# Kernel optimization log

Hardware: AMD Instinct MI355X
Metric: run time of the kernel (lower is better)

The kernel has to match this reference:

```python
import jax, jax.numpy as jnp
import numpy as np

KP_EXTENT = 1.2  # influence radius of each kernel point (init arg KP_extent)
SHADOW_COORD = 1e6  # shadow point coordinate for padding (as in original KPConv)


def setup_inputs() -> dict:
    key = jax.random.key(0)
    k1, k2, k3, k4, k5, k6 = jax.random.split(key, 6)
    N, Ns, H, K, Cin, Cout = 20000, 20000, 40, 15, 128, 128
    q_pts = jax.random.uniform(k1, (N, 3), dtype=jnp.float32)
    s_pts = jax.random.uniform(k2, (Ns, 3), dtype=jnp.float32)
    neighb_inds = jax.random.randint(k3, (N, H), 0, Ns, dtype=jnp.int32)
    x = jax.random.normal(k4, (Ns, Cin), dtype=jnp.float32)
    # kernel point positions inside the sphere (stand-in for load_kernels output)
    kernel_points = jax.random.normal(k5, (K, 3), dtype=jnp.float32) * 0.5
    kernel_points = kernel_points.at[0].set(0.0)  # fixed='center'
    weights = jax.random.normal(k6, (K, Cin, Cout), dtype=jnp.float32) * (1.0 / np.sqrt(Cin))
    return {"q_pts": q_pts, "s_pts": s_pts, "neighb_inds": neighb_inds,
            "x": x, "kernel_points": kernel_points, "weights": weights}


def reference(q_pts, s_pts, neighb_inds, x, kernel_points, weights):
    # Pad support points with a far-away shadow point and features with a zero row,
    # so out-of-range neighbor index Ns contributes nothing (original KPConv trick).
    s_pad = jnp.concatenate([s_pts, jnp.full((1, s_pts.shape[1]), SHADOW_COORD, s_pts.dtype)], axis=0)
    x_pad = jnp.concatenate([x, jnp.zeros((1, x.shape[1]), x.dtype)], axis=0)

    # Gather neighbor coords, center on query points: [N, H, 3]
    neighbors = s_pad[neighb_inds] - q_pts[:, None, :]

    # Squared distance to every kernel point: [N, H, K]
    diff = neighbors[:, :, None, :] - kernel_points[None, None, :, :]
    sq_dist = jnp.sum(diff * diff, axis=-1)

    # Linear influence weights, aggregation_mode='sum': [N, K, H]
    all_weights = jnp.clip(1.0 - jnp.sqrt(sq_dist) / KP_EXTENT, 0.0, None)
    all_weights = jnp.swapaxes(all_weights, 1, 2)

    # Gather neighbor features: [N, H, Cin]
    neighb_x = x_pad[neighb_inds]

    # Influence-weighted aggregation over neighbors: [N, K, Cin]
    weighted = jnp.einsum('nkh,nhc->nkc', all_weights, neighb_x)

    # Per-kernel-point linear maps, summed over kernel points: [N, Cout]
    out = jnp.einsum('nkc,kcd->nd', weighted, weights)
    return out
```

## Files before the change

kernel.cpp:

```cpp
#include <hip/hip_runtime.h>

#define KP   15
#define HN   40
#define CIN  128
#define COUT 128
#define KDIM (KP*CIN)
#define KP_EXT_INV (1.0f/1.2f)

typedef __bf16 bf16x8 __attribute__((ext_vector_type(8)));
typedef __bf16 bf16x4 __attribute__((ext_vector_type(4)));
typedef float  f32x4  __attribute__((ext_vector_type(4)));

__device__ inline void async_copy16(const void* g, void* lds) {
    __builtin_amdgcn_global_load_lds(
        (const __attribute__((address_space(1))) unsigned int*)g,
        (__attribute__((address_space(3))) unsigned int*)lds, 16, 0, 0);
}

__global__ __launch_bounds__(256)
void kpconv_prep(const float* __restrict__ x, const float* __restrict__ W,
                 __bf16* __restrict__ xb, __bf16* __restrict__ Wt,
                 int nx_elems, int nxB)
{
    __shared__ float sW[32][133];
    const int b = blockIdx.x;
    const int t = threadIdx.x;

    if (b < nxB) {
        const int e0 = (b*256 + t) * 8;
        if (e0 + 8 <= nx_elems) {
            const float4 f0 = *(const float4*)(x + e0);
            const float4 f1 = *(const float4*)(x + e0 + 4);
            bf16x8 v;
            v[0]=(__bf16)f0.x; v[1]=(__bf16)f0.y; v[2]=(__bf16)f0.z; v[3]=(__bf16)f0.w;
            v[4]=(__bf16)f1.x; v[5]=(__bf16)f1.y; v[6]=(__bf16)f1.z; v[7]=(__bf16)f1.w;
            *(bf16x8*)(xb + e0) = v;
        } else {
            for (int e = e0; e < nx_elems; ++e) xb[e] = (__bf16)x[e];
        }
    } else {
        const int kc0 = (b - nxB) * 32;
        #pragma unroll
        for (int i = 0; i < 4; ++i) {
            const int off = t*4 + i*1024;
            const int r = off >> 7, c = off & 127;
            const float4 f = *(const float4*)(W + (size_t)(kc0 + r)*COUT + c);
            sW[r][c+0]=f.x; sW[r][c+1]=f.y; sW[r][c+2]=f.z; sW[r][c+3]=f.w;
        }
        __syncthreads();
        #pragma unroll
        for (int i = 0; i < 2; ++i) {
            const int id = t + i*256;
            const int d  = id >> 2, ch = id & 3;
            bf16x8 v;
            #pragma unroll
            for (int j = 0; j < 8; ++j) v[j] = (__bf16)sW[ch*8 + j][d];
            *(bf16x8*)(Wt + (size_t)d*KDIM + kc0 + ch*8) = v;
        }
    }
}

__global__ __launch_bounds__(256, 4)
void kpconv_aggregate(const float* __restrict__ q_pts,
                      const float* __restrict__ s_pts,
                      const int*   __restrict__ nb,
                      const __bf16* __restrict__ xb,
                      const float* __restrict__ kpts,
                      __bf16* __restrict__ wsA,
                      int N, int Ns)
{
    __shared__ __align__(16) __bf16 sXt[4][4][128][8];
    __shared__ __align__(16) float4 s_nd[4][HN];
    __shared__ int                  s_idx[4][HN];

    const int t  = threadIdx.x;
    const int wv = t >> 6;
    const int l  = t & 63;
    const int m  = l & 15;
    const int q  = l >> 4;
    const int n  = blockIdx.x * 4 + wv;

    if (l < HN) {
        int idx = nb[n*HN + l];
        float dx, dy, dz;
        if (idx >= 0 && idx < Ns) {
            dx = s_pts[idx*3+0] - q_pts[n*3+0];
            dy = s_pts[idx*3+1] - q_pts[n*3+1];
            dz = s_pts[idx*3+2] - q_pts[n*3+2];
        } else { idx = 0; dx = dy = dz = 2.0e6f; }
        s_idx[wv][l] = idx;
        s_nd[wv][l]  = make_float4(dx, dy, dz, 0.f);
    }
    __asm__ __volatile__("s_waitcnt lgkmcnt(0)" ::: "memory");

    float kx = 0.f, ky = 0.f, kz = 0.f;
    if (m < KP) { kx = kpts[m*3+0]; ky = kpts[m*3+1]; kz = kpts[m*3+2]; }

    bf16x8 wfrag[2];
    #pragma unroll
    for (int ks = 0; ks < 2; ++ks) {
        #pragma unroll
        for (int j = 0; j < 8; ++j) {
            const int h = ks*32 + q*8 + j;
            float w = 0.f;
            if (m < KP && h < HN) {
                float4 nd = s_nd[wv][h];
                float dx = nd.x - kx, dy = nd.y - ky, dz = nd.z - kz;
                w = fmaxf(1.0f - sqrtf(dx*dx + dy*dy + dz*dz)*KP_EXT_INV, 0.f);
            }
            wfrag[ks][j] = (__bf16)w;
        }
    }

    f32x4 acc[8];
    #pragma unroll
    for (int nt = 0; nt < 8; ++nt) acc[nt] = (f32x4){0.f,0.f,0.f,0.f};

    #pragma unroll
    for (int ks = 0; ks < 2; ++ks) {
        const int iters = ks ? 1 : 4;
        #pragma unroll
        for (int it = 0; it < iters; ++it) {
            const int hp = ks*16 + it*4 + q;
            const int h0 = 2*hp;
            const uint4 a  = *(const uint4*)(xb + (size_t)s_idx[wv][h0  ]*CIN + m*8);
            const uint4 bb = *(const uint4*)(xb + (size_t)s_idx[wv][h0+1]*CIN + m*8);
            const unsigned av[4] = {a.x, a.y, a.z, a.w};
            const unsigned bv[4] = {bb.x, bb.y, bb.z, bb.w};
            const int hl = h0 - ks*32;
            const int hc = hl >> 3;
            const int dw = hp & 3;
            unsigned* plane = (unsigned*)&sXt[wv][hc][0][0];
            #pragma unroll
            for (int j = 0; j < 8; ++j) {
                const unsigned v = __builtin_amdgcn_perm(
                    bv[j>>1], av[j>>1], (j&1) ? 0x07060302u : 0x05040100u);
                const int p = m*8 + (j ^ (m & 7));
                plane[p*4 + dw] = v;
            }
        }
        __asm__ __volatile__("s_waitcnt lgkmcnt(0)" ::: "memory");

        #pragma unroll
        for (int nt = 0; nt < 8; ++nt) {
            const int cc = nt*16 + m;
            const int p  = (cc & ~7) | ((cc & 7) ^ ((cc >> 3) & 7));
            bf16x8 xf = *(const bf16x8*)&sXt[wv][q][p][0];
            acc[nt] = __builtin_amdgcn_mfma_f32_16x16x32_bf16(
                          xf, wfrag[ks], acc[nt], 0, 0, 0);
        }
    }

    if (m < KP) {
        #pragma unroll
        for (int nt = 0; nt < 8; ++nt) {
            bf16x4 v;
            #pragma unroll
            for (int r = 0; r < 4; ++r) v[r] = (__bf16)acc[nt][r];
            *(bf16x4*)(wsA + (size_t)n*KDIM + m*CIN + nt*16 + q*4) = v;
        }
    }
}

#define BM 64
#define BK 128

__global__ __launch_bounds__(256, 3)
void kpconv_gemm(const __bf16* __restrict__ A,
                 const __bf16* __restrict__ Bt,
                 float* __restrict__ out, int M)
{
    __shared__ __align__(16) __bf16 sA[BM*BK];
    __shared__ __align__(16) __bf16 sB[COUT*BK];

    const int t     = threadIdx.x;
    const int wv    = t >> 6;
    const int l     = t & 63;
    const int mlane = l & 15;
    const int q     = l >> 4;
    const int m0    = blockIdx.x * BM;

    const int rA = t >> 4;
    const int pA = t & 15;

    f32x4 acc[4][2];
    #pragma unroll
    for (int i = 0; i < 4; ++i)
        #pragma unroll
        for (int j = 0; j < 2; ++j) acc[i][j] = (f32x4){0.f,0.f,0.f,0.f};

    for (int k0 = 0; k0 < KDIM; k0 += BK) {
        #pragma unroll
        for (int pass = 0; pass < 4; ++pass) {
            const int r  = rA + pass*16;
            int rg = m0 + r; if (rg >= M) rg = M - 1;
            const int ch = pA ^ (r & 15);
            async_copy16(A + (size_t)rg*KDIM + k0 + ch*8,
                         (char*)sA + pass*4096 + wv*1024 + l*16);
        }
        #pragma unroll
        for (int pass = 0; pass < 8; ++pass) {
            const int r  = rA + pass*16;
            const int ch = pA ^ (r & 15);
            async_copy16(Bt + (size_t)r*KDIM + k0 + ch*8,
                         (char*)sB + pass*4096 + wv*1024 + l*16);
        }
        __syncthreads();

        #pragma unroll
        for (int ksi = 0; ksi < 4; ++ksi) {
            bf16x8 af[4], bfr[2];
            #pragma unroll
            for (int mt = 0; mt < 4; ++mt) {
                const int row = mt*16 + mlane;
                const int p   = (ksi*4 + q) ^ (row & 15);
                af[mt] = *(const bf16x8*)&sA[row*BK + p*8];
            }
            #pragma unroll
            for (int j = 0; j < 2; ++j) {
                const int row = (wv*2 + j)*16 + mlane;
                const int p   = (ksi*4 + q) ^ (row & 15);
                bfr[j] = *(const bf16x8*)&sB[row*BK + p*8];
            }
            #pragma unroll
            for (int mt = 0; mt < 4; ++mt)
                #pragma unroll
                for (int j = 0; j < 2; ++j)
                    acc[mt][j] = __builtin_amdgcn_mfma_f32_16x16x32_bf16(
                                     af[mt], bfr[j], acc[mt][j], 0, 0, 0);
        }
        __syncthreads();
    }

    #pragma unroll
    for (int mt = 0; mt < 4; ++mt)
        #pragma unroll
        for (int j = 0; j < 2; ++j)
            #pragma unroll
            for (int r = 0; r < 4; ++r) {
                const int row = m0 + mt*16 + q*4 + r;
                if (row < M)
                    out[(size_t)row*COUT + (wv*2+j)*16 + mlane] = acc[mt][j][r];
            }
}

#define TM 8
#define WSTR (KP*CIN + 4)

__global__ __launch_bounds__(256, 2)
void kpconv_fused(const float* __restrict__ q_pts,
                  const float* __restrict__ s_pts,
                  const int*   __restrict__ nb,
                  const float* __restrict__ x,
                  const float* __restrict__ kpts,
                  const float* __restrict__ W,
                  float* __restrict__ out,
                  int N, int Ns)
{
    __shared__ float s_kp[KP*3];
    __shared__ float s_nd2[HN*3];
    __shared__ int   s_idx2[HN];
    __shared__ float s_w[KP][HN];
    __shared__ float s_wt[TM*WSTR];

    const int t  = threadIdx.x;
    const int n0 = (int)blockIdx.x * TM;
    if (t < KP*3) s_kp[t] = kpts[t];
    const int c = t & (CIN-1);
    const int g = t >> 7;

    for (int mm = 0; mm < TM; ++mm) {
        const int n = n0 + mm;
        if (t < HN) {
            float dx = 1e6f, dy = 1e6f, dz = 1e6f;
            int idx = 0;
            if (n < N) {
                idx = nb[n*HN + t];
                if (idx >= 0 && idx < Ns) {
                    dx = s_pts[idx*3+0] - q_pts[n*3+0];
                    dy = s_pts[idx*3+1] - q_pts[n*3+1];
                    dz = s_pts[idx*3+2] - q_pts[n*3+2];
                } else idx = 0;
            }
            s_idx2[t] = idx;
            s_nd2[t*3+0] = dx; s_nd2[t*3+1] = dy; s_nd2[t*3+2] = dz;
        }
        __syncthreads();
        for (int task = t; task < KP*HN; task += 256) {
            const int k = task / HN;
            const int h = task - k*HN;
            const float dx = s_nd2[h*3+0] - s_kp[k*3+0];
            const float dy = s_nd2[h*3+1] - s_kp[k*3+1];
            const float dz = s_nd2[h*3+2] - s_kp[k*3+2];
            s_w[k][h] = fmaxf(1.0f - sqrtf(dx*dx+dy*dy+dz*dz)*KP_EXT_INV, 0.0f);
        }
        __syncthreads();
        float facc[8];
        #pragma unroll
        for (int j = 0; j < 8; ++j) facc[j] = 0.0f;
        #pragma unroll 8
        for (int h = 0; h < HN; ++h) {
            const float xv = x[s_idx2[h]*CIN + c];
            #pragma unroll
            for (int j = 0; j < 8; ++j) {
                const int k = g + 2*j;
                if (k < KP) facc[j] += s_w[k][h] * xv;
            }
        }
        #pragma unroll
        for (int j = 0; j < 8; ++j) {
            const int k = g + 2*j;
            if (k < KP) s_wt[mm*WSTR + k*CIN + c] = facc[j];
        }
        __syncthreads();
    }

    const int m3 = t >> 5;
    const int d0 = (t & 31) * 4;
    const float* wm = &s_wt[m3*WSTR];
    float ax = 0.f, ay = 0.f, az = 0.f, aw = 0.f;
    #pragma unroll 4
    for (int kc = 0; kc < KP*CIN; ++kc) {
        const float  wvv = wm[kc];
        const float4 wr = *(const float4*)&W[kc*COUT + d0];
        ax += wvv * wr.x; ay += wvv * wr.y; az += wvv * wr.z; aw += wvv * wr.w;
    }
    const int n = n0 + m3;
    if (n < N) {
        float4 o; o.x = ax; o.y = ay; o.z = az; o.w = aw;
        *(float4*)&out[n*COUT + d0] = o;
    }
}

extern "C" void kernel_launch(void* const* d_in, const int* in_sizes, int n_in,
                              void* d_out, int out_size, void* d_ws, size_t ws_size,
                              hipStream_t stream) {
    const float* q_pts = (const float*)d_in[0];
    const float* s_pts = (const float*)d_in[1];
    const int*   nb    = (const int*)  d_in[2];
    const float* x     = (const float*)d_in[3];
    const float* kpts  = (const float*)d_in[4];
    const float* W     = (const float*)d_in[5];
    float* out = (float*)d_out;

    const int N  = in_sizes[0] / 3;
    const int Ns = in_sizes[1] / 3;
    const int nx = in_sizes[3];

    const size_t needA = (size_t)N * KDIM * sizeof(__bf16);
    const size_t needB = (size_t)COUT * KDIM * sizeof(__bf16);
    const size_t needX = (size_t)nx * sizeof(__bf16);

    if (ws_size >= needA + needB + needX && (N % 4) == 0 && (KDIM % 128) == 0) {
        __bf16* wsA = (__bf16*)d_ws;
        __bf16* wsB = (__bf16*)((char*)d_ws + needA);
        __bf16* wsX = (__bf16*)((char*)d_ws + needA + needB);

        const int nxB = (nx/8 + 255) / 256;
        const int nwB = KDIM / 32;
        hipLaunchKernelGGL(kpconv_prep, dim3(nxB + nwB), dim3(256), 0, stream,
                           x, W, wsX, wsB, nx, nxB);
        hipLaunchKernelGGL(kpconv_aggregate, dim3(N/4), dim3(256), 0, stream,
                           q_pts, s_pts, nb, wsX, kpts, wsA, N, Ns);
        hipLaunchKernelGGL(kpconv_gemm, dim3((N + BM - 1)/BM), dim3(256), 0, stream,
                           wsA, wsB, out, N);
    } else {
        const int grid = (N + TM - 1) / TM;
        hipLaunchKernelGGL(kpconv_fused, dim3(grid), dim3(256), 0, stream,
                           q_pts, s_pts, nb, x, kpts, W, out, N, Ns);
    }
}
```

Measured before the change: 148.2 us.

## Process two points per wave with prefetched gathers; shrink GEMM tile, read B from registers

The aggregate kernel now handles two query points per wave. It issues all neighbor feature gathers for both points up front into registers, so their latency overlaps the influence-weight computation, and it rewrites the squared distance as a precomputed-norm fma form using a fast sqrt. The GEMM drops its LDS staging of the weight matrix, loading B fragments straight from global memory (expected to hit L2), and halves the M tile to 32 rows so more blocks run. The costs are higher register pressure in the aggregate kernel (launch bounds lowered to 3), repeated global reads of B per block, and a new requirement that N be divisible by 32.

```diff
diff --git a/kernel.cpp b/kernel.cpp
--- a/kernel.cpp
+++ b/kernel.cpp
@@ -16,6 +16,7 @@
         (const __attribute__((address_space(1))) unsigned int*)g,
         (__attribute__((address_space(3))) unsigned int*)lds, 16, 0, 0);
 }
+#define LGKM0() __asm__ __volatile__("s_waitcnt lgkmcnt(0)" ::: "memory")
 
 __global__ __launch_bounds__(256)
 void kpconv_prep(const float* __restrict__ x, const float* __restrict__ W,
@@ -60,7 +61,7 @@
     }
 }
 
-__global__ __launch_bounds__(256, 4)
+__global__ __launch_bounds__(256, 3)
 void kpconv_aggregate(const float* __restrict__ q_pts,
                       const float* __restrict__ s_pts,
                       const int*   __restrict__ nb,
@@ -70,178 +71,195 @@
                       int N, int Ns)
 {
     __shared__ __align__(16) __bf16 sXt[4][4][128][8];
-    __shared__ __align__(16) float4 s_nd[4][HN];
-    __shared__ int                  s_idx[4][HN];
+    __shared__ __align__(16) float4 s_nd[4][2][HN];
+    __shared__ int                  s_idx[4][2][HN];
 
     const int t  = threadIdx.x;
     const int wv = t >> 6;
     const int l  = t & 63;
     const int m  = l & 15;
     const int q  = l >> 4;
-    const int n  = blockIdx.x * 4 + wv;
-
-    if (l < HN) {
-        int idx = nb[n*HN + l];
-        float dx, dy, dz;
-        if (idx >= 0 && idx < Ns) {
-            dx = s_pts[idx*3+0] - q_pts[n*3+0];
-            dy = s_pts[idx*3+1] - q_pts[n*3+1];
-            dz = s_pts[idx*3+2] - q_pts[n*3+2];
-        } else { idx = 0; dx = dy = dz = 2.0e6f; }
-        s_idx[wv][l] = idx;
-        s_nd[wv][l]  = make_float4(dx, dy, dz, 0.f);
-    }
-    __asm__ __volatile__("s_waitcnt lgkmcnt(0)" ::: "memory");
-
-    float kx = 0.f, ky = 0.f, kz = 0.f;
+    const int nbase = (blockIdx.x*4 + wv)*2;
+
+    #pragma unroll
+    for (int pp = 0; pp < 2; ++pp) {
+        if (l < HN) {
+            const int n = nbase + pp;
+            int idx = nb[n*HN + l];
+            float dx, dy, dz;
+            if (idx >= 0 && idx < Ns) {
+                dx = s_pts[idx*3+0] - q_pts[n*3+0];
+                dy = s_pts[idx*3+1] - q_pts[n*3+1];
+                dz = s_pts[idx*3+2] - q_pts[n*3+2];
+            } else { idx = 0; dx = dy = dz = 2.0e6f; }
+            s_idx[wv][pp][l] = idx;
+            s_nd[wv][pp][l]  = make_float4(dx, dy, dz, dx*dx + dy*dy + dz*dz);
+        }
+    }
+    LGKM0();
+
+    uint4 g[2][5][2];
+    #pragma unroll
+    for (int pp = 0; pp < 2; ++pp) {
+        #pragma unroll
+        for (int it = 0; it < 5; ++it) {
+            const int h0 = (it < 4) ? (it*8 + 2*q) : (32 + 2*q);
+            g[pp][it][0] = *(const uint4*)(xb + (size_t)s_idx[wv][pp][h0  ]*CIN + m*8);
+            g[pp][it][1] = *(const uint4*)(xb + (size_t)s_idx[wv][pp][h0+1]*CIN + m*8);
+        }
+    }
+
+    float kx=0.f, ky=0.f, kz=0.f;
     if (m < KP) { kx = kpts[m*3+0]; ky = kpts[m*3+1]; kz = kpts[m*3+2]; }
-
-    bf16x8 wfrag[2];
-    #pragma unroll
-    for (int ks = 0; ks < 2; ++ks) {
-        #pragma unroll
-        for (int j = 0; j < 8; ++j) {
-            const int h = ks*32 + q*8 + j;
-            float w = 0.f;
-            if (m < KP && h < HN) {
-                float4 nd = s_nd[wv][h];
-                float dx = nd.x - kx, dy = nd.y - ky, dz = nd.z - kz;
-                w = fmaxf(1.0f - sqrtf(dx*dx + dy*dy + dz*dz)*KP_EXT_INV, 0.f);
-            }
-            wfrag[ks][j] = (__bf16)w;
-        }
-    }
-
-    f32x4 acc[8];
-    #pragma unroll
-    for (int nt = 0; nt < 8; ++nt) acc[nt] = (f32x4){0.f,0.f,0.f,0.f};
-
-    #pragma unroll
-    for (int ks = 0; ks < 2; ++ks) {
-        const int iters = ks ? 1 : 4;
-        #pragma unroll
-        for (int it = 0; it < iters; ++it) {
-            const int hp = ks*16 + it*4 + q;
-            const int h0 = 2*hp;
-            const uint4 a  = *(const uint4*)(xb + (size_t)s_idx[wv][h0  ]*CIN + m*8);
-            const uint4 bb = *(const uint4*)(xb + (size_t)s_idx[wv][h0+1]*CIN + m*8);
-            const unsigned av[4] = {a.x, a.y, a.z, a.w};
-            const unsigned bv[4] = {bb.x, bb.y, bb.z, bb.w};
-            const int hl = h0 - ks*32;
-            const int hc = hl >> 3;
-            const int dw = hp & 3;
-            unsigned* plane = (unsigned*)&sXt[wv][hc][0][0];
+    const float kk  = kx*kx + ky*ky + kz*kz;
+    const float kx2 = -2.f*kx, ky2 = -2.f*ky, kz2 = -2.f*kz;
+
+    bf16x8 wfrag[2][2];
+    #pragma unroll
+    for (int pp = 0; pp < 2; ++pp) {
+        #pragma unroll
+        for (int ks = 0; ks < 2; ++ks) {
             #pragma unroll
             for (int j = 0; j < 8; ++j) {
-                const unsigned v = __builtin_amdgcn_perm(
-                    bv[j>>1], av[j>>1], (j&1) ? 0x07060302u : 0x05040100u);
-                const int p = m*8 + (j ^ (m & 7));
-                plane[p*4 + dw] = v;
-            }
-        }
-        __asm__ __volatile__("s_waitcnt lgkmcnt(0)" ::: "memory");
-
-        #pragma unroll
-        for (int nt = 0; nt < 8; ++nt) {
-            const int cc = nt*16 + m;
-            const int p  = (cc & ~7) | ((cc & 7) ^ ((cc >> 3) & 7));
-            bf16x8 xf = *(const bf16x8*)&sXt[wv][q][p][0];
-            acc[nt] = __builtin_amdgcn_mfma_f32_16x16x32_bf16(
-                          xf, wfrag[ks], acc[nt], 0, 0, 0);
-        }
-    }
-
-    if (m < KP) {
-        #pragma unroll
-        for (int nt = 0; nt < 8; ++nt) {
-            bf16x4 v;
-            #pragma unroll
-            for (int r = 0; r < 4; ++r) v[r] = (__bf16)acc[nt][r];
-            *(bf16x4*)(wsA + (size_t)n*KDIM + m*CIN + nt*16 + q*4) = v;
-        }
-    }
-}
-
-#define BM 64
-#define BK 128
-
-__global__ __launch_bounds__(256, 3)
+                const int h = ks*32 + q*8 + j;
+                float w = 0.f;
+                if (m < KP && h < HN) {
+                    const float4 nd = s_nd[wv][pp][h];
+                    const float d2 = fmaf(nd.x, kx2,
+                                     fmaf(nd.y, ky2,
+                                     fmaf(nd.z, kz2, nd.w + kk)));
+                    const float d = __builtin_amdgcn_sqrtf(d2);
+                    w = fmaxf(fmaf(d, -KP_EXT_INV, 1.0f), 0.f);
+                }
+                wfrag[pp][ks][j] = (__bf16)w;
+            }
+        }
+    }
+
+    #pragma unroll
+    for (int pp = 0; pp < 2; ++pp) {
+        const int n = nbase + pp;
+        f32x4 acc[8];
+        #pragma unroll
+        for (int nt = 0; nt < 8; ++nt) acc[nt] = (f32x4){0.f,0.f,0.f,0.f};
+
+        #pragma unroll
+        for (int ks = 0; ks < 2; ++ks) {
+            const int itBeg = ks ? 4 : 0;
+            const int itEnd = ks ? 5 : 4;
+            #pragma unroll
+            for (int it = itBeg; it < itEnd; ++it) {
+                const unsigned av[4] = {g[pp][it][0].x, g[pp][it][0].y,
+                                        g[pp][it][0].z, g[pp][it][0].w};
+                const unsigned bv[4] = {g[pp][it][1].x, g[pp][it][1].y,
+                                        g[pp][it][1].z, g[pp][it][1].w};
+                const int hc = ks ? 0 : it;
+                const int dw = q;
+                unsigned* plane = (unsigned*)&sXt[wv][hc][0][0];
+                #pragma unroll
+                for (int j = 0; j < 8; ++j) {
+                    const unsigned v = __builtin_amdgcn_perm(
+                        bv[j>>1], av[j>>1], (j&1) ? 0x07060302u : 0x05040100u);
+                    const int p = m*8 + (j ^ (m & 7));
+                    plane[p*4 + dw] = v;
+                }
+            }
+            LGKM0();
+
+            #pragma unroll
+            for (int nt = 0; nt < 8; ++nt) {
+                const int cc = nt*16 + m;
+                const int p  = (cc & ~7) | ((cc & 7) ^ ((cc >> 3) & 7));
+                bf16x8 xf = *(const bf16x8*)&sXt[wv][q][p][0];
+                acc[nt] = __builtin_amdgcn_mfma_f32_16x16x32_bf16(
+                              xf, wfrag[pp][ks], acc[nt], 0, 0, 0);
+            }
+        }
+
+        if (m < KP) {
+            #pragma unroll
+            for (int nt = 0; nt < 8; ++nt) {
+                bf16x4 v;
+                #pragma unroll
+                for (int r = 0; r < 4; ++r) v[r] = (__bf16)acc[nt][r];
+                *(bf16x4*)(wsA + (size_t)n*KDIM + m*CIN + nt*16 + q*4) = v;
+            }
+        }
+    }
+}
+
+#define GBM 32
+
+__global__ __launch_bounds__(256, 4)
 void kpconv_gemm(const __bf16* __restrict__ A,
                  const __bf16* __restrict__ Bt,
                  float* __restrict__ out, int M)
 {
-    __shared__ __align__(16) __bf16 sA[BM*BK];
-    __shared__ __align__(16) __bf16 sB[COUT*BK];
+    __shared__ __align__(16) __bf16 sA[GBM*128];
 
     const int t     = threadIdx.x;
     const int wv    = t >> 6;
     const int l     = t & 63;
     const int mlane = l & 15;
     const int q     = l >> 4;
-    const int m0    = blockIdx.x * BM;
-
-    const int rA = t >> 4;
-    const int pA = t & 15;
-
-    f32x4 acc[4][2];
-    #pragma unroll
-    for (int i = 0; i < 4; ++i)
+    const int m0    = blockIdx.x * GBM;
+
+    const int r0  = t >> 4;
+    const int pos = t & 15;
+
+    const __bf16* Brow0 = Bt + (size_t)(wv*32 + mlane) * KDIM;
+    const __bf16* Brow1 = Brow0 + (size_t)16 * KDIM;
+
+    f32x4 acc[2][2];
+    #pragma unroll
+    for (int i = 0; i < 2; ++i)
         #pragma unroll
         for (int j = 0; j < 2; ++j) acc[i][j] = (f32x4){0.f,0.f,0.f,0.f};
 
-    for (int k0 = 0; k0 < KDIM; k0 += BK) {
-        #pragma unroll
-        for (int pass = 0; pass < 4; ++pass) {
-            const int r  = rA + pass*16;
-            int rg = m0 + r; if (rg >= M) rg = M - 1;
-            const int ch = pA ^ (r & 15);
-            async_copy16(A + (size_t)rg*KDIM + k0 + ch*8,
-                         (char*)sA + pass*4096 + wv*1024 + l*16);
-        }
-        #pragma unroll
-        for (int pass = 0; pass < 8; ++pass) {
-            const int r  = rA + pass*16;
-            const int ch = pA ^ (r & 15);
-            async_copy16(Bt + (size_t)r*KDIM + k0 + ch*8,
-                         (char*)sB + pass*4096 + wv*1024 + l*16);
-        }
-        __syncthreads();
-
-        #pragma unroll
-        for (int ksi = 0; ksi < 4; ++ksi) {
-            bf16x8 af[4], bfr[2];
-            #pragma unroll
-            for (int mt = 0; mt < 4; ++mt) {
+    for (int k0 = 0; k0 < KDIM; k0 += 128) {
+        #pragma unroll
+        for (int p = 0; p < 2; ++p) {
+            const int row = r0 + p*16;
+            const int ch  = pos ^ (row & 15);
+            async_copy16(A + (size_t)(m0 + row)*KDIM + k0 + ch*8,
+                         (char*)sA + (p*256 + t)*16);
+        }
+        __syncthreads();
+
+        bf16x8 bfr[2][4];
+        #pragma unroll
+        for (int ks = 0; ks < 4; ++ks) {
+            bfr[0][ks] = *(const bf16x8*)(Brow0 + k0 + ks*32 + q*8);
+            bfr[1][ks] = *(const bf16x8*)(Brow1 + k0 + ks*32 + q*8);
+        }
+
+        #pragma unroll
+        for (int ks = 0; ks < 4; ++ks) {
+            bf16x8 af[2];
+            #pragma unroll
+            for (int mt = 0; mt < 2; ++mt) {
                 const int row = mt*16 + mlane;
-                const int p   = (ksi*4 + q) ^ (row & 15);
-                af[mt] = *(const bf16x8*)&sA[row*BK + p*8];
-            }
-            #pragma unroll
-            for (int j = 0; j < 2; ++j) {
-                const int row = (wv*2 + j)*16 + mlane;
-                const int p   = (ksi*4 + q) ^ (row & 15);
-                bfr[j] = *(const bf16x8*)&sB[row*BK + p*8];
-            }
-            #pragma unroll
-            for (int mt = 0; mt < 4; ++mt)
+                const int p   = (ks*4 + q) ^ (row & 15);
+                af[mt] = *(const bf16x8*)&sA[row*128 + p*8];
+            }
+            #pragma unroll
+            for (int mt = 0; mt < 2; ++mt)
                 #pragma unroll
                 for (int j = 0; j < 2; ++j)
                     acc[mt][j] = __builtin_amdgcn_mfma_f32_16x16x32_bf16(
-                                     af[mt], bfr[j], acc[mt][j], 0, 0, 0);
-        }
-        __syncthreads();
-    }
-
-    #pragma unroll
-    for (int mt = 0; mt < 4; ++mt)
+                                     af[mt], bfr[j][ks], acc[mt][j], 0, 0, 0);
+        }
+        __syncthreads();
+    }
+
+    #pragma unroll
+    for (int mt = 0; mt < 2; ++mt)
         #pragma unroll
         for (int j = 0; j < 2; ++j)
             #pragma unroll
-            for (int r = 0; r < 4; ++r) {
-                const int row = m0 + mt*16 + q*4 + r;
-                if (row < M)
-                    out[(size_t)row*COUT + (wv*2+j)*16 + mlane] = acc[mt][j][r];
-            }
+            for (int r = 0; r < 4; ++r)
+                out[(size_t)(m0 + mt*16 + q*4 + r)*COUT + wv*32 + j*16 + mlane]
+                    = acc[mt][j][r];
 }
 
 #define TM 8
@@ -351,7 +369,8 @@
     const size_t needB = (size_t)COUT * KDIM * sizeof(__bf16);
     const size_t needX = (size_t)nx * sizeof(__bf16);
 
-    if (ws_size >= needA + needB + needX && (N % 4) == 0 && (KDIM % 128) == 0) {
+    if (ws_size >= needA + needB + needX && (N % 8) == 0 && (N % GBM) == 0
+        && (KDIM % 128) == 0) {
         __bf16* wsA = (__bf16*)d_ws;
         __bf16* wsB = (__bf16*)((char*)d_ws + needA);
         __bf16* wsX = (__bf16*)((char*)d_ws + needA + needB);
@@ -360,9 +379,9 @@
         const int nwB = KDIM / 32;
         hipLaunchKernelGGL(kpconv_prep, dim3(nxB + nwB), dim3(256), 0, stream,
                            x, W, wsX, wsB, nx, nxB);
-        hipLaunchKernelGGL(kpconv_aggregate, dim3(N/4), dim3(256), 0, stream,
+        hipLaunchKernelGGL(kpconv_aggregate, dim3(N/8), dim3(256), 0, stream,
                            q_pts, s_pts, nb, wsX, kpts, wsA, N, Ns);
-        hipLaunchKernelGGL(kpconv_gemm, dim3((N + BM - 1)/BM), dim3(256), 0, stream,
+        hipLaunchKernelGGL(kpconv_gemm, dim3(N/GBM), dim3(256), 0, stream,
                            wsA, wsB, out, N);
     } else {
         const int grid = (N + TM - 1) / TM;
```

Measured after the change: 164.9 us. +11.2%, slower.
